# Kernel tuning notes

Hardware: AMD Instinct MI355X
Metric: run time of the kernel (lower is better)

Reference implementation:

```python
import jax, jax.numpy as jnp
import numpy as np

B, T_ENC, T_DEC = 8, 256, 256
ENC_DIM, DEC_UNITS = 512, 256


def setup_inputs() -> dict:
    key = jax.random.key(0)
    ks = jax.random.split(key, 6)
    s1 = 1.0 / np.sqrt(ENC_DIM)
    s2 = 1.0 / np.sqrt(DEC_UNITS)
    return {
        "enc_outputs": jax.random.normal(ks[0], (B, T_ENC, ENC_DIM), jnp.float32),
        "dec_outputs": jax.random.normal(ks[1], (B, T_DEC, DEC_UNITS), jnp.float32),
        "W1": jax.random.normal(ks[2], (ENC_DIM, DEC_UNITS), jnp.float32) * s1,
        "b1": jnp.zeros((DEC_UNITS,), jnp.float32),
        "W2": jax.random.normal(ks[3], (DEC_UNITS, DEC_UNITS), jnp.float32) * s2,
        "b2": jnp.zeros((DEC_UNITS,), jnp.float32),
        "Vw": jax.random.normal(ks[4], (DEC_UNITS,), jnp.float32) * s2,
        "Vb": jnp.zeros((1,), jnp.float32),
    }


def reference(enc_outputs, dec_outputs, W1, b1, W2, b2, Vw, Vb):
    # proj_enc: (B, T_enc, U); proj_dec: (B, T_dec, U)
    proj_enc = jnp.einsum("bte,eu->btu", enc_outputs, W1) + b1
    proj_dec = jnp.einsum("bsd,du->bsu", dec_outputs, W2) + b2
    # broadcast add -> (B, T_dec, T_enc, U), tanh, then contract with Vw -> score (B, T_dec, T_enc)
    hidden = jnp.tanh(proj_dec[:, :, None, :] + proj_enc[:, None, :, :])
    score = jnp.einsum("bstu,u->bst", hidden, Vw) + Vb[0]
    attention_weights = jax.nn.softmax(score, axis=-1)
    # context: (B, T_dec, enc_dim)
    context = jnp.einsum("bst,bte->bse", attention_weights, enc_outputs)
    return (context, attention_weights)
```

## Files before the change

kernel.cpp:

```cpp
#include <hip/hip_runtime.h>

#define NB 8
#define TE 256
#define TD 256
#define ED 512
#define DU 256


__global__ __launch_bounds__(512) void proj_exp_kernel(
    const float* __restrict__ enc, const float* __restrict__ dec,
    const float* __restrict__ W1, const float* __restrict__ b1,
    const float* __restrict__ W2, const float* __restrict__ b2,
    float* __restrict__ Epd, float* __restrict__ EpeT2)
{
  __shared__ __align__(16) float As[2][32][34];
  __shared__ __align__(16) float Bs[2][32][64];
  __shared__ __align__(16) float comb[8][256];
  const int blk = blockIdx.x;
  const bool is_pe = blk < 256;
  const int sub = blk & 255;
  const int K = is_pe ? ED : DU;
  const int NTh = K >> 6;
  const float* __restrict__ A = is_pe ? enc : dec;
  const float* __restrict__ W = is_pe ? W1 : W2;
  const float* __restrict__ bias = is_pe ? b1 : b2;
  const int mt = sub >> 2, nt = sub & 3;
  const int m0 = mt * 32, n0 = nt * 64;
  const int tid = threadIdx.x;
  const int t = tid & 255;
  const int h = tid >> 8;
  const int k0base = h * (K >> 1);
  const int tx = t & 15, ty = t >> 4;
  const int at = t >> 3, ka = (t & 7) << 2;
  const int kb = t >> 4, jb = (t & 15) << 2;

  const float* __restrict__ Ap = A + (size_t)(m0 + at) * K + k0base + ka;
  const float* __restrict__ Wp = W + (size_t)(k0base + kb) * DU + n0 + jb;

  float acc[2][4] = {};
  float4 aV, wV0, wV1;

  auto loadr = [&](int k0) {
    aV = *(const float4*)(Ap + k0);
    wV0 = *(const float4*)(Wp + (size_t)k0 * DU);
    wV1 = *(const float4*)(Wp + (size_t)(k0 + 16) * DU);
  };

  loadr(0);
  for (int kt = 0; kt < NTh; ++kt) {
    As[h][ka + 0][at] = aV.x;
    As[h][ka + 1][at] = aV.y;
    As[h][ka + 2][at] = aV.z;
    As[h][ka + 3][at] = aV.w;
    *(float4*)&Bs[h][kb][jb] = wV0;
    *(float4*)&Bs[h][kb + 16][jb] = wV1;
    __syncthreads();
    if (kt + 1 < NTh) loadr((kt + 1) << 5);
#pragma unroll
    for (int kk = 0; kk < 32; ++kk) {
      const float2 a2 = *(const float2*)&As[h][kk][ty * 2];
      const float4 w4 = *(const float4*)&Bs[h][kk][tx * 4];
      acc[0][0] = fmaf(a2.x, w4.x, acc[0][0]);
      acc[0][1] = fmaf(a2.x, w4.y, acc[0][1]);
      acc[0][2] = fmaf(a2.x, w4.z, acc[0][2]);
      acc[0][3] = fmaf(a2.x, w4.w, acc[0][3]);
      acc[1][0] = fmaf(a2.y, w4.x, acc[1][0]);
      acc[1][1] = fmaf(a2.y, w4.y, acc[1][1]);
      acc[1][2] = fmaf(a2.y, w4.z, acc[1][2]);
      acc[1][3] = fmaf(a2.y, w4.w, acc[1][3]);
    }
    __syncthreads();
  }

  if (h == 1) {
#pragma unroll
    for (int r = 0; r < 2; ++r)
#pragma unroll
      for (int j = 0; j < 4; ++j) comb[r * 4 + j][t] = acc[r][j];
  }
  __syncthreads();
  if (h == 0) {
#pragma unroll
    for (int r = 0; r < 2; ++r)
#pragma unroll
      for (int j = 0; j < 4; ++j) acc[r][j] += comb[r * 4 + j][t];

    const float4 bv4 = *(const float4*)(bias + n0 + tx * 4);
    const float bvv[4] = {bv4.x, bv4.y, bv4.z, bv4.w};
    if (is_pe) {
      const int b = m0 >> 8, t0 = m0 & 255;
      const int uqg = (b << 6) + (n0 >> 2) + tx;
      const int tg = t0 + ty * 2;
      float* dst = EpeT2 + ((size_t)uqg << 10) + (tg << 2);
      float4 o0, o1;
      o0.x = __expf(2.0f * (acc[0][0] + bvv[0]));
      o0.y = __expf(2.0f * (acc[0][1] + bvv[1]));
      o0.z = __expf(2.0f * (acc[0][2] + bvv[2]));
      o0.w = __expf(2.0f * (acc[0][3] + bvv[3]));
      o1.x = __expf(2.0f * (acc[1][0] + bvv[0]));
      o1.y = __expf(2.0f * (acc[1][1] + bvv[1]));
      o1.z = __expf(2.0f * (acc[1][2] + bvv[2]));
      o1.w = __expf(2.0f * (acc[1][3] + bvv[3]));
      *(float4*)dst = o0;
      *(float4*)(dst + 4) = o1;
    } else {
#pragma unroll
      for (int r = 0; r < 2; ++r) {
        const int m = m0 + ty * 2 + r;
        float4 o;
        o.x = __expf(2.0f * (acc[r][0] + bvv[0]));
        o.y = __expf(2.0f * (acc[r][1] + bvv[1]));
        o.z = __expf(2.0f * (acc[r][2] + bvv[2]));
        o.w = __expf(2.0f * (acc[r][3] + bvv[3]));
        *(float4*)(Epd + ((size_t)m << 8) + n0 + tx * 4) = o;
      }
    }
  }
}

__global__ __launch_bounds__(512) void score_ctx_kernel(
    const float* __restrict__ Epd, const float* __restrict__ EpeT2,
    const float* __restrict__ Vw, const float* __restrict__ enc,
    float* __restrict__ attn, float* __restrict__ ctx)
{
  __shared__ __align__(16) float eps[4 * 256];
  __shared__ __align__(16) float vws[256];
  __shared__ __align__(16) float comb[4][256];
  __shared__ __align__(16) float att[4][256];
  __shared__ float redm[4][4];
  __shared__ float reds[4][4];

  const int blk0 = blockIdx.x;
  const int blk = ((blk0 & 7) << 6) | (blk0 >> 3);
  const int b = blk >> 6;
  const int s0 = (blk & 63) << 2;
  const int tid = threadIdx.x;
  const int t = tid & 255;
  const int h = tid >> 8;

  if (h == 0) {
    ((float4*)eps)[t] =
        ((const float4*)(Epd + (((size_t)((b << 8) + s0)) << 8)))[t];
  } else if (t < 64) {
    ((float4*)vws)[t] = ((const float4*)Vw)[t];
  }
  __syncthreads();

  const float* __restrict__ ep =
      EpeT2 + ((size_t)b << 16) + ((size_t)h << 15) + (t << 2);
  const int qb = h << 5;

  float a0 = 0.f, a1 = 0.f, a2 = 0.f, a3 = 0.f;
  float4 g = *(const float4*)ep;
#pragma unroll 4
  for (int q = 0; q < 32; ++q) {
    float4 gn;
    if (q + 1 < 32) gn = *(const float4*)(ep + ((size_t)(q + 1) << 10));
    const int u4 = (qb + q) << 2;
    const float4 vw = *(const float4*)&vws[u4];
    const float4 e0 = *(const float4*)&eps[u4];
    const float4 e1 = *(const float4*)&eps[256 + u4];
    const float4 e2 = *(const float4*)&eps[512 + u4];
    const float4 e3 = *(const float4*)&eps[768 + u4];
    a0 = fmaf(vw.x, __builtin_amdgcn_rcpf(fmaf(e0.x, g.x, 1.0f)), a0);
    a1 = fmaf(vw.x, __builtin_amdgcn_rcpf(fmaf(e1.x, g.x, 1.0f)), a1);
    a2 = fmaf(vw.x, __builtin_amdgcn_rcpf(fmaf(e2.x, g.x, 1.0f)), a2);
    a3 = fmaf(vw.x, __builtin_amdgcn_rcpf(fmaf(e3.x, g.x, 1.0f)), a3);
    a0 = fmaf(vw.y, __builtin_amdgcn_rcpf(fmaf(e0.y, g.y, 1.0f)), a0);
    a1 = fmaf(vw.y, __builtin_amdgcn_rcpf(fmaf(e1.y, g.y, 1.0f)), a1);
    a2 = fmaf(vw.y, __builtin_amdgcn_rcpf(fmaf(e2.y, g.y, 1.0f)), a2);
    a3 = fmaf(vw.y, __builtin_amdgcn_rcpf(fmaf(e3.y, g.y, 1.0f)), a3);
    a0 = fmaf(vw.z, __builtin_amdgcn_rcpf(fmaf(e0.z, g.z, 1.0f)), a0);
    a1 = fmaf(vw.z, __builtin_amdgcn_rcpf(fmaf(e1.z, g.z, 1.0f)), a1);
    a2 = fmaf(vw.z, __builtin_amdgcn_rcpf(fmaf(e2.z, g.z, 1.0f)), a2);
    a3 = fmaf(vw.z, __builtin_amdgcn_rcpf(fmaf(e3.z, g.z, 1.0f)), a3);
    a0 = fmaf(vw.w, __builtin_amdgcn_rcpf(fmaf(e0.w, g.w, 1.0f)), a0);
    a1 = fmaf(vw.w, __builtin_amdgcn_rcpf(fmaf(e1.w, g.w, 1.0f)), a1);
    a2 = fmaf(vw.w, __builtin_amdgcn_rcpf(fmaf(e2.w, g.w, 1.0f)), a2);
    a3 = fmaf(vw.w, __builtin_amdgcn_rcpf(fmaf(e3.w, g.w, 1.0f)), a3);
    g = gn;
  }

  if (h == 1) {
    comb[0][t] = a0;
    comb[1][t] = a1;
    comb[2][t] = a2;
    comb[3][t] = a3;
  }
  __syncthreads();

  const int wid = tid >> 6, lane = tid & 63;
  float v[4], e[4];
  if (h == 0) {
    v[0] = -2.f * (a0 + comb[0][t]);
    v[1] = -2.f * (a1 + comb[1][t]);
    v[2] = -2.f * (a2 + comb[2][t]);
    v[3] = -2.f * (a3 + comb[3][t]);
#pragma unroll
    for (int r = 0; r < 4; ++r) {
      float m = v[r];
#pragma unroll
      for (int off = 32; off; off >>= 1) m = fmaxf(m, __shfl_xor(m, off));
      if (lane == 0) redm[r][wid] = m;
    }
  }
  __syncthreads();
  if (h == 0) {
#pragma unroll
    for (int r = 0; r < 4; ++r) {
      const float m = fmaxf(fmaxf(redm[r][0], redm[r][1]),
                            fmaxf(redm[r][2], redm[r][3]));
      e[r] = __expf(v[r] - m);
      float s = e[r];
#pragma unroll
      for (int off = 32; off; off >>= 1) s += __shfl_xor(s, off);
      if (lane == 0) reds[r][wid] = s;
    }
  }
  __syncthreads();
  if (h == 0) {
#pragma unroll
    for (int r = 0; r < 4; ++r) {
      const float s = (reds[r][0] + reds[r][1]) + (reds[r][2] + reds[r][3]);
      const float p = e[r] * __builtin_amdgcn_rcpf(s);
      attn[(((size_t)((b << 8) + s0 + r)) << 8) + t] = p;
      att[r][t] = p;
    }
  }
  __syncthreads();

  const int c = tid;
  const float* __restrict__ encb = enc + ((size_t)b << 17) + c;
  float acc0 = 0.f, acc1 = 0.f, acc2 = 0.f, acc3 = 0.f;
#pragma unroll 2
  for (int t0 = 0; t0 < 256; t0 += 4) {
    const float4 p0 = *(const float4*)&att[0][t0];
    const float4 p1 = *(const float4*)&att[1][t0];
    const float4 p2 = *(const float4*)&att[2][t0];
    const float4 p3 = *(const float4*)&att[3][t0];
    const float pv0[4] = {p0.x, p0.y, p0.z, p0.w};
    const float pv1[4] = {p1.x, p1.y, p1.z, p1.w};
    const float pv2[4] = {p2.x, p2.y, p2.z, p2.w};
    const float pv3[4] = {p3.x, p3.y, p3.z, p3.w};
#pragma unroll
    for (int i = 0; i < 4; ++i) {
      const float ev = encb[(size_t)(t0 + i) << 9];
      acc0 = fmaf(pv0[i], ev, acc0);
      acc1 = fmaf(pv1[i], ev, acc1);
      acc2 = fmaf(pv2[i], ev, acc2);
      acc3 = fmaf(pv3[i], ev, acc3);
    }
  }
  float* __restrict__ cb = ctx + (((size_t)((b << 8) + s0)) << 9) + c;
  cb[0 * ED] = acc0;
  cb[1 * ED] = acc1;
  cb[2 * ED] = acc2;
  cb[3 * ED] = acc3;
}

extern "C" void kernel_launch(void* const* d_in, const int* in_sizes, int n_in,
                              void* d_out, int out_size, void* d_ws, size_t ws_size,
                              hipStream_t stream) {
  const float* enc = (const float*)d_in[0];
  const float* dec = (const float*)d_in[1];
  const float* W1 = (const float*)d_in[2];
  const float* b1 = (const float*)d_in[3];
  const float* W2 = (const float*)d_in[4];
  const float* b2 = (const float*)d_in[5];
  const float* Vw = (const float*)d_in[6];

  float* ctx = (float*)d_out;
  float* attn = (float*)d_out + (size_t)NB * TD * ED;
  float* Epd = (float*)d_ws;
  float* EpeT2 = Epd + (size_t)NB * TD * DU;

  proj_exp_kernel<<<dim3(512), dim3(512), 0, stream>>>(enc, dec, W1, b1, W2,
                                                       b2, Epd, EpeT2);
  score_ctx_kernel<<<dim3(512), dim3(512), 0, stream>>>(Epd, EpeT2, Vw, enc,
                                                        attn, ctx);
}
```

Baseline: 53.91 us.

## Pair reciprocals, read operands from global, drop softmax max pass

The score loop now combines two tanh reciprocal terms into one reciprocal of their product, halving the rcp instructions. The decoder projection and Vw values are read straight from global (cached) memory instead of being staged in shared memory, which removes a barrier. The softmax max-reduction pass and its barrier are dropped, relying on the scores being bounded so exp cannot overflow. This risks precision loss if the product A*B overflows or underflows, and assumes bounded scores in place of the usual stabilisation.

```diff
diff --git a/kernel.cpp b/kernel.cpp
--- a/kernel.cpp
+++ b/kernel.cpp
@@ -123,11 +123,8 @@
     const float* __restrict__ Vw, const float* __restrict__ enc,
     float* __restrict__ attn, float* __restrict__ ctx)
 {
-  __shared__ __align__(16) float eps[4 * 256];
-  __shared__ __align__(16) float vws[256];
   __shared__ __align__(16) float comb[4][256];
   __shared__ __align__(16) float att[4][256];
-  __shared__ float redm[4][4];
   __shared__ float reds[4][4];
 
   const int blk0 = blockIdx.x;
@@ -138,14 +135,9 @@
   const int t = tid & 255;
   const int h = tid >> 8;
 
-  if (h == 0) {
-    ((float4*)eps)[t] =
-        ((const float4*)(Epd + (((size_t)((b << 8) + s0)) << 8)))[t];
-  } else if (t < 64) {
-    ((float4*)vws)[t] = ((const float4*)Vw)[t];
-  }
-  __syncthreads();
-
+  const float4* __restrict__ pd4 =
+      (const float4*)(Epd + (((size_t)((b << 8) + s0)) << 8));
+  const float4* __restrict__ vw4 = (const float4*)Vw;
   const float* __restrict__ ep =
       EpeT2 + ((size_t)b << 16) + ((size_t)h << 15) + (t << 2);
   const int qb = h << 5;
@@ -156,28 +148,52 @@
   for (int q = 0; q < 32; ++q) {
     float4 gn;
     if (q + 1 < 32) gn = *(const float4*)(ep + ((size_t)(q + 1) << 10));
-    const int u4 = (qb + q) << 2;
-    const float4 vw = *(const float4*)&vws[u4];
-    const float4 e0 = *(const float4*)&eps[u4];
-    const float4 e1 = *(const float4*)&eps[256 + u4];
-    const float4 e2 = *(const float4*)&eps[512 + u4];
-    const float4 e3 = *(const float4*)&eps[768 + u4];
-    a0 = fmaf(vw.x, __builtin_amdgcn_rcpf(fmaf(e0.x, g.x, 1.0f)), a0);
-    a1 = fmaf(vw.x, __builtin_amdgcn_rcpf(fmaf(e1.x, g.x, 1.0f)), a1);
-    a2 = fmaf(vw.x, __builtin_amdgcn_rcpf(fmaf(e2.x, g.x, 1.0f)), a2);
-    a3 = fmaf(vw.x, __builtin_amdgcn_rcpf(fmaf(e3.x, g.x, 1.0f)), a3);
-    a0 = fmaf(vw.y, __builtin_amdgcn_rcpf(fmaf(e0.y, g.y, 1.0f)), a0);
-    a1 = fmaf(vw.y, __builtin_amdgcn_rcpf(fmaf(e1.y, g.y, 1.0f)), a1);
-    a2 = fmaf(vw.y, __builtin_amdgcn_rcpf(fmaf(e2.y, g.y, 1.0f)), a2);
-    a3 = fmaf(vw.y, __builtin_amdgcn_rcpf(fmaf(e3.y, g.y, 1.0f)), a3);
-    a0 = fmaf(vw.z, __builtin_amdgcn_rcpf(fmaf(e0.z, g.z, 1.0f)), a0);
-    a1 = fmaf(vw.z, __builtin_amdgcn_rcpf(fmaf(e1.z, g.z, 1.0f)), a1);
-    a2 = fmaf(vw.z, __builtin_amdgcn_rcpf(fmaf(e2.z, g.z, 1.0f)), a2);
-    a3 = fmaf(vw.z, __builtin_amdgcn_rcpf(fmaf(e3.z, g.z, 1.0f)), a3);
-    a0 = fmaf(vw.w, __builtin_amdgcn_rcpf(fmaf(e0.w, g.w, 1.0f)), a0);
-    a1 = fmaf(vw.w, __builtin_amdgcn_rcpf(fmaf(e1.w, g.w, 1.0f)), a1);
-    a2 = fmaf(vw.w, __builtin_amdgcn_rcpf(fmaf(e2.w, g.w, 1.0f)), a2);
-    a3 = fmaf(vw.w, __builtin_amdgcn_rcpf(fmaf(e3.w, g.w, 1.0f)), a3);
+    const int qq = qb + q;
+    const float4 vw = vw4[qq];
+    const float4 e0 = pd4[qq];
+    const float4 e1 = pd4[64 + qq];
+    const float4 e2 = pd4[128 + qq];
+    const float4 e3 = pd4[192 + qq];
+    {
+      const float A = fmaf(e0.x, g.x, 1.0f), B = fmaf(e0.y, g.y, 1.0f);
+      float n = vw.x * B;
+      n = fmaf(vw.y, A, n);
+      a0 = fmaf(n, __builtin_amdgcn_rcpf(A * B), a0);
+      const float C = fmaf(e0.z, g.z, 1.0f), D = fmaf(e0.w, g.w, 1.0f);
+      float n2 = vw.z * D;
+      n2 = fmaf(vw.w, C, n2);
+      a0 = fmaf(n2, __builtin_amdgcn_rcpf(C * D), a0);
+    }
+    {
+      const float A = fmaf(e1.x, g.x, 1.0f), B = fmaf(e1.y, g.y, 1.0f);
+      float n = vw.x * B;
+      n = fmaf(vw.y, A, n);
+      a1 = fmaf(n, __builtin_amdgcn_rcpf(A * B), a1);
+      const float C = fmaf(e1.z, g.z, 1.0f), D = fmaf(e1.w, g.w, 1.0f);
+      float n2 = vw.z * D;
+      n2 = fmaf(vw.w, C, n2);
+      a1 = fmaf(n2, __builtin_amdgcn_rcpf(C * D), a1);
+    }
+    {
+      const float A = fmaf(e2.x, g.x, 1.0f), B = fmaf(e2.y, g.y, 1.0f);
+      float n = vw.x * B;
+      n = fmaf(vw.y, A, n);
+      a2 = fmaf(n, __builtin_amdgcn_rcpf(A * B), a2);
+      const float C = fmaf(e2.z, g.z, 1.0f), D = fmaf(e2.w, g.w, 1.0f);
+      float n2 = vw.z * D;
+      n2 = fmaf(vw.w, C, n2);
+      a2 = fmaf(n2, __builtin_amdgcn_rcpf(C * D), a2);
+    }
+    {
+      const float A = fmaf(e3.x, g.x, 1.0f), B = fmaf(e3.y, g.y, 1.0f);
+      float n = vw.x * B;
+      n = fmaf(vw.y, A, n);
+      a3 = fmaf(n, __builtin_amdgcn_rcpf(A * B), a3);
+      const float C = fmaf(e3.z, g.z, 1.0f), D = fmaf(e3.w, g.w, 1.0f);
+      float n2 = vw.z * D;
+      n2 = fmaf(vw.w, C, n2);
+      a3 = fmaf(n2, __builtin_amdgcn_rcpf(C * D), a3);
+    }
     g = gn;
   }
 
@@ -190,27 +206,13 @@
   __syncthreads();
 
   const int wid = tid >> 6, lane = tid & 63;
-  float v[4], e[4];
+  float e[4];
   if (h == 0) {
-    v[0] = -2.f * (a0 + comb[0][t]);
-    v[1] = -2.f * (a1 + comb[1][t]);
-    v[2] = -2.f * (a2 + comb[2][t]);
-    v[3] = -2.f * (a3 + comb[3][t]);
 #pragma unroll
     for (int r = 0; r < 4; ++r) {
-      float m = v[r];
-#pragma unroll
-      for (int off = 32; off; off >>= 1) m = fmaxf(m, __shfl_xor(m, off));
-      if (lane == 0) redm[r][wid] = m;
-    }
-  }
-  __syncthreads();
-  if (h == 0) {
-#pragma unroll
-    for (int r = 0; r < 4; ++r) {
-      const float m = fmaxf(fmaxf(redm[r][0], redm[r][1]),
-                            fmaxf(redm[r][2], redm[r][3]));
-      e[r] = __expf(v[r] - m);
+      const float v =
+          -2.f * ((r == 0 ? a0 : r == 1 ? a1 : r == 2 ? a2 : a3) + comb[r][t]);
+      e[r] = __expf(v);
       float s = e[r];
 #pragma unroll
       for (int off = 32; off; off >>= 1) s += __shfl_xor(s, off);
```

Measured after the change: 60.05 us. 1.11x slower.

## Double score/context block threads and drop the softmax max-reduction pass

Applied to the files above, without the earlier changes.

The score/context kernel now runs 1024 threads per block instead of 512. The U-dimension reduction is split four ways and merged through shared memory, and the context accumulation over encoder time is split in two and merged the same way. The softmax max-subtraction pass and one barrier are removed, relying on the score being bounded by the tanh range. The goal is more parallel work per block to hide memory latency. The cost is extra shared-memory traffic and barriers, tighter register limits from the launch bounds, and less numerical safety in the softmax.

```diff
diff --git a/kernel.cpp b/kernel.cpp
--- a/kernel.cpp
+++ b/kernel.cpp
@@ -118,16 +118,16 @@
   }
 }
 
-__global__ __launch_bounds__(512) void score_ctx_kernel(
+__global__ __launch_bounds__(1024, 8) void score_ctx_kernel(
     const float* __restrict__ Epd, const float* __restrict__ EpeT2,
     const float* __restrict__ Vw, const float* __restrict__ enc,
     float* __restrict__ attn, float* __restrict__ ctx)
 {
   __shared__ __align__(16) float eps[4 * 256];
   __shared__ __align__(16) float vws[256];
-  __shared__ __align__(16) float comb[4][256];
+  __shared__ __align__(16) float comb[3][4][256];
   __shared__ __align__(16) float att[4][256];
-  __shared__ float redm[4][4];
+  __shared__ __align__(16) float ctx2[4][512];
   __shared__ float reds[4][4];
 
   const int blk0 = blockIdx.x;
@@ -136,26 +136,26 @@
   const int s0 = (blk & 63) << 2;
   const int tid = threadIdx.x;
   const int t = tid & 255;
-  const int h = tid >> 8;
-
-  if (h == 0) {
+  const int hq = tid >> 8;
+
+  if (hq == 0) {
     ((float4*)eps)[t] =
         ((const float4*)(Epd + (((size_t)((b << 8) + s0)) << 8)))[t];
-  } else if (t < 64) {
+  } else if (hq == 1 && t < 64) {
     ((float4*)vws)[t] = ((const float4*)Vw)[t];
   }
   __syncthreads();
 
+  const int qb = hq << 4;
   const float* __restrict__ ep =
-      EpeT2 + ((size_t)b << 16) + ((size_t)h << 15) + (t << 2);
-  const int qb = h << 5;
+      EpeT2 + ((size_t)b << 16) + ((size_t)qb << 10) + (t << 2);
 
   float a0 = 0.f, a1 = 0.f, a2 = 0.f, a3 = 0.f;
   float4 g = *(const float4*)ep;
 #pragma unroll 4
-  for (int q = 0; q < 32; ++q) {
+  for (int q = 0; q < 16; ++q) {
     float4 gn;
-    if (q + 1 < 32) gn = *(const float4*)(ep + ((size_t)(q + 1) << 10));
+    if (q + 1 < 16) gn = *(const float4*)(ep + ((size_t)(q + 1) << 10));
     const int u4 = (qb + q) << 2;
     const float4 vw = *(const float4*)&vws[u4];
     const float4 e0 = *(const float4*)&eps[u4];
@@ -181,36 +181,25 @@
     g = gn;
   }
 
-  if (h == 1) {
-    comb[0][t] = a0;
-    comb[1][t] = a1;
-    comb[2][t] = a2;
-    comb[3][t] = a3;
+  if (hq != 0) {
+    comb[hq - 1][0][t] = a0;
+    comb[hq - 1][1][t] = a1;
+    comb[hq - 1][2][t] = a2;
+    comb[hq - 1][3][t] = a3;
   }
   __syncthreads();
 
   const int wid = tid >> 6, lane = tid & 63;
-  float v[4], e[4];
-  if (h == 0) {
-    v[0] = -2.f * (a0 + comb[0][t]);
-    v[1] = -2.f * (a1 + comb[1][t]);
-    v[2] = -2.f * (a2 + comb[2][t]);
-    v[3] = -2.f * (a3 + comb[3][t]);
+  float e[4];
+  if (hq == 0) {
+    float vv[4];
+    vv[0] = a0 + comb[0][0][t] + comb[1][0][t] + comb[2][0][t];
+    vv[1] = a1 + comb[0][1][t] + comb[1][1][t] + comb[2][1][t];
+    vv[2] = a2 + comb[0][2][t] + comb[1][2][t] + comb[2][2][t];
+    vv[3] = a3 + comb[0][3][t] + comb[1][3][t] + comb[2][3][t];
 #pragma unroll
     for (int r = 0; r < 4; ++r) {
-      float m = v[r];
-#pragma unroll
-      for (int off = 32; off; off >>= 1) m = fmaxf(m, __shfl_xor(m, off));
-      if (lane == 0) redm[r][wid] = m;
-    }
-  }
-  __syncthreads();
-  if (h == 0) {
-#pragma unroll
-    for (int r = 0; r < 4; ++r) {
-      const float m = fmaxf(fmaxf(redm[r][0], redm[r][1]),
-                            fmaxf(redm[r][2], redm[r][3]));
-      e[r] = __expf(v[r] - m);
+      e[r] = __expf(-2.f * vv[r]);
       float s = e[r];
 #pragma unroll
       for (int off = 32; off; off >>= 1) s += __shfl_xor(s, off);
@@ -218,7 +207,7 @@
     }
   }
   __syncthreads();
-  if (h == 0) {
+  if (hq == 0) {
 #pragma unroll
     for (int r = 0; r < 4; ++r) {
       const float s = (reds[r][0] + reds[r][1]) + (reds[r][2] + reds[r][3]);
@@ -229,11 +218,13 @@
   }
   __syncthreads();
 
-  const int c = tid;
+  const int c = tid & 511;
+  const int h2 = tid >> 9;
+  const int tb = h2 << 7;
   const float* __restrict__ encb = enc + ((size_t)b << 17) + c;
   float acc0 = 0.f, acc1 = 0.f, acc2 = 0.f, acc3 = 0.f;
 #pragma unroll 2
-  for (int t0 = 0; t0 < 256; t0 += 4) {
+  for (int t0 = tb; t0 < tb + 128; t0 += 4) {
     const float4 p0 = *(const float4*)&att[0][t0];
     const float4 p1 = *(const float4*)&att[1][t0];
     const float4 p2 = *(const float4*)&att[2][t0];
@@ -251,11 +242,24 @@
       acc3 = fmaf(pv3[i], ev, acc3);
     }
   }
-  float* __restrict__ cb = ctx + (((size_t)((b << 8) + s0)) << 9) + c;
-  cb[0 * ED] = acc0;
-  cb[1 * ED] = acc1;
-  cb[2 * ED] = acc2;
-  cb[3 * ED] = acc3;
+  if (h2 == 1) {
+    ctx2[0][c] = acc0;
+    ctx2[1][c] = acc1;
+    ctx2[2][c] = acc2;
+    ctx2[3][c] = acc3;
+  }
+  __syncthreads();
+  if (h2 == 0) {
+    acc0 += ctx2[0][c];
+    acc1 += ctx2[1][c];
+    acc2 += ctx2[2][c];
+    acc3 += ctx2[3][c];
+    float* __restrict__ cb = ctx + (((size_t)((b << 8) + s0)) << 9) + c;
+    cb[0 * ED] = acc0;
+    cb[1 * ED] = acc1;
+    cb[2 * ED] = acc2;
+    cb[3 * ED] = acc3;
+  }
 }
 
 extern "C" void kernel_launch(void* const* d_in, const int* in_sizes, int n_in,
@@ -276,6 +280,6 @@
 
   proj_exp_kernel<<<dim3(512), dim3(512), 0, stream>>>(enc, dec, W1, b1, W2,
                                                        b2, Epd, EpeT2);
-  score_ctx_kernel<<<dim3(512), dim3(512), 0, stream>>>(Epd, EpeT2, Vw, enc,
-                                                        attn, ctx);
+  score_ctx_kernel<<<dim3(512), dim3(1024), 0, stream>>>(Epd, EpeT2, Vw, enc,
+                                                         attn, ctx);
 }
```

Result: slower. 97.73 us (+81.3%).

## Drop softmax max pass and split context reduction across T with float4 loads

Applied to the files above, without the earlier changes.

The softmax no longer subtracts the row max. The score is a bounded tanh sum, so exp is taken directly, which removes one reduction pass and one barrier. The context product now has each thread load float4 encoder rows over a quarter of the T range. Partial sums are combined through a new 24KB shared buffer and written as float4. This adds shared memory, which may lower occupancy, and relies on the scores being bounded so that exp stays stable.

```diff
diff --git a/kernel.cpp b/kernel.cpp
--- a/kernel.cpp
+++ b/kernel.cpp
@@ -127,7 +127,7 @@
   __shared__ __align__(16) float vws[256];
   __shared__ __align__(16) float comb[4][256];
   __shared__ __align__(16) float att[4][256];
-  __shared__ float redm[4][4];
+  __shared__ __align__(16) float ctx2[3][4][512];
   __shared__ float reds[4][4];
 
   const int blk0 = blockIdx.x;
@@ -190,27 +190,16 @@
   __syncthreads();
 
   const int wid = tid >> 6, lane = tid & 63;
-  float v[4], e[4];
+  float e[4];
   if (h == 0) {
-    v[0] = -2.f * (a0 + comb[0][t]);
-    v[1] = -2.f * (a1 + comb[1][t]);
-    v[2] = -2.f * (a2 + comb[2][t]);
-    v[3] = -2.f * (a3 + comb[3][t]);
+    float vv[4];
+    vv[0] = a0 + comb[0][t];
+    vv[1] = a1 + comb[1][t];
+    vv[2] = a2 + comb[2][t];
+    vv[3] = a3 + comb[3][t];
 #pragma unroll
     for (int r = 0; r < 4; ++r) {
-      float m = v[r];
-#pragma unroll
-      for (int off = 32; off; off >>= 1) m = fmaxf(m, __shfl_xor(m, off));
-      if (lane == 0) redm[r][wid] = m;
-    }
-  }
-  __syncthreads();
-  if (h == 0) {
-#pragma unroll
-    for (int r = 0; r < 4; ++r) {
-      const float m = fmaxf(fmaxf(redm[r][0], redm[r][1]),
-                            fmaxf(redm[r][2], redm[r][3]));
-      e[r] = __expf(v[r] - m);
+      e[r] = __expf(-2.f * vv[r]);
       float s = e[r];
 #pragma unroll
       for (int off = 32; off; off >>= 1) s += __shfl_xor(s, off);
@@ -229,11 +218,16 @@
   }
   __syncthreads();
 
-  const int c = tid;
-  const float* __restrict__ encb = enc + ((size_t)b << 17) + c;
-  float acc0 = 0.f, acc1 = 0.f, acc2 = 0.f, acc3 = 0.f;
+  const int c4 = (tid & 127) << 2;
+  const int tq = tid >> 7;
+  const int tb = tq << 6;
+  const float* __restrict__ encb = enc + ((size_t)b << 17) + c4;
+  float4 acc0 = {0.f, 0.f, 0.f, 0.f};
+  float4 acc1 = {0.f, 0.f, 0.f, 0.f};
+  float4 acc2 = {0.f, 0.f, 0.f, 0.f};
+  float4 acc3 = {0.f, 0.f, 0.f, 0.f};
 #pragma unroll 2
-  for (int t0 = 0; t0 < 256; t0 += 4) {
+  for (int t0 = tb; t0 < tb + 64; t0 += 4) {
     const float4 p0 = *(const float4*)&att[0][t0];
     const float4 p1 = *(const float4*)&att[1][t0];
     const float4 p2 = *(const float4*)&att[2][t0];
@@ -244,18 +238,50 @@
     const float pv3[4] = {p3.x, p3.y, p3.z, p3.w};
 #pragma unroll
     for (int i = 0; i < 4; ++i) {
-      const float ev = encb[(size_t)(t0 + i) << 9];
-      acc0 = fmaf(pv0[i], ev, acc0);
-      acc1 = fmaf(pv1[i], ev, acc1);
-      acc2 = fmaf(pv2[i], ev, acc2);
-      acc3 = fmaf(pv3[i], ev, acc3);
-    }
-  }
-  float* __restrict__ cb = ctx + (((size_t)((b << 8) + s0)) << 9) + c;
-  cb[0 * ED] = acc0;
-  cb[1 * ED] = acc1;
-  cb[2 * ED] = acc2;
-  cb[3 * ED] = acc3;
+      const float4 ev = *(const float4*)(encb + ((size_t)(t0 + i) << 9));
+      acc0.x = fmaf(pv0[i], ev.x, acc0.x);
+      acc0.y = fmaf(pv0[i], ev.y, acc0.y);
+      acc0.z = fmaf(pv0[i], ev.z, acc0.z);
+      acc0.w = fmaf(pv0[i], ev.w, acc0.w);
+      acc1.x = fmaf(pv1[i], ev.x, acc1.x);
+      acc1.y = fmaf(pv1[i], ev.y, acc1.y);
+      acc1.z = fmaf(pv1[i], ev.z, acc1.z);
+      acc1.w = fmaf(pv1[i], ev.w, acc1.w);
+      acc2.x = fmaf(pv2[i], ev.x, acc2.x);
+      acc2.y = fmaf(pv2[i], ev.y, acc2.y);
+      acc2.z = fmaf(pv2[i], ev.z, acc2.z);
+      acc2.w = fmaf(pv2[i], ev.w, acc2.w);
+      acc3.x = fmaf(pv3[i], ev.x, acc3.x);
+      acc3.y = fmaf(pv3[i], ev.y, acc3.y);
+      acc3.z = fmaf(pv3[i], ev.z, acc3.z);
+      acc3.w = fmaf(pv3[i], ev.w, acc3.w);
+    }
+  }
+  if (tq != 0) {
+    *(float4*)&ctx2[tq - 1][0][c4] = acc0;
+    *(float4*)&ctx2[tq - 1][1][c4] = acc1;
+    *(float4*)&ctx2[tq - 1][2][c4] = acc2;
+    *(float4*)&ctx2[tq - 1][3][c4] = acc3;
+  }
+  __syncthreads();
+  if (tq == 0) {
+#pragma unroll
+    for (int q = 0; q < 3; ++q) {
+      const float4 q0 = *(const float4*)&ctx2[q][0][c4];
+      const float4 q1 = *(const float4*)&ctx2[q][1][c4];
+      const float4 q2 = *(const float4*)&ctx2[q][2][c4];
+      const float4 q3 = *(const float4*)&ctx2[q][3][c4];
+      acc0.x += q0.x; acc0.y += q0.y; acc0.z += q0.z; acc0.w += q0.w;
+      acc1.x += q1.x; acc1.y += q1.y; acc1.z += q1.z; acc1.w += q1.w;
+      acc2.x += q2.x; acc2.y += q2.y; acc2.z += q2.z; acc2.w += q2.w;
+      acc3.x += q3.x; acc3.y += q3.y; acc3.z += q3.z; acc3.w += q3.w;
+    }
+    float* __restrict__ cb = ctx + (((size_t)((b << 8) + s0)) << 9) + c4;
+    *(float4*)(cb + 0 * ED) = acc0;
+    *(float4*)(cb + 1 * ED) = acc1;
+    *(float4*)(cb + 2 * ED) = acc2;
+    *(float4*)(cb + 3 * ED) = acc3;
+  }
 }
 
 extern "C" void kernel_launch(void* const* d_in, const int* in_sizes, int n_in,
```

Measured after the change: 48.32 us. 1.12x faster.
